# Kernel tuning notes

Measured on AMD Instinct MI355X. Metric: run time of the kernel, lower is better.

## Reference

```python
import jax, jax.numpy as jnp
import numpy as np
from jax import lax

B, N, C = 8, 4096, 384
HEADS = 6


def setup_inputs() -> dict:
    key = jax.random.key(0)
    ks = jax.random.split(key, 10)
    d = C // HEADS
    return {
        "x": jax.random.normal(ks[0], (B, N, C), jnp.float32),
        "q_w": jax.random.normal(ks[1], (C, C), jnp.float32) * 0.02,
        "q_b": jnp.zeros((C,), jnp.float32),
        "kv_w": jax.random.normal(ks[2], (2 * C, C), jnp.float32) * 0.02,
        "kv_b": jnp.zeros((2 * C,), jnp.float32),
        "fc_w": jax.random.normal(ks[3], (9, 3 * HEADS, 1, 1), jnp.float32) * 0.33,
        "fc_b": jnp.zeros((9,), jnp.float32),
        "dep_w": jax.random.normal(ks[4], (C, 9, 3, 3), jnp.float32) * 0.15,
        "dep_b": jnp.zeros((C,), jnp.float32),
        "ln_g": jnp.ones((C,), jnp.float32),
        "ln_b": jnp.zeros((C,), jnp.float32),
        "proj_w": jax.random.normal(ks[5], (C, C), jnp.float32) * 0.02,
        "proj_b": jnp.zeros((C,), jnp.float32),
        "H": 64,
        "W": 64,
    }


def reference(x, q_w, q_b, kv_w, kv_b, fc_w, fc_b, dep_w, dep_b, ln_g, ln_b, proj_w, proj_b, H, W):
    b, n, c = x.shape
    heads = fc_w.shape[1] // 3
    d = c // heads  # head dim == conv groups
    # QKV projections
    q = x @ q_w.T + q_b                                    # [B,N,C]
    kv = x @ kv_w.T + kv_b                                 # [B,N,2C]
    kv_ = kv.reshape(b, n, 2 * heads, d).transpose(0, 2, 1, 3)  # [B,2h,N,d]
    qh = q.reshape(b, n, heads, d).transpose(0, 2, 1, 3)        # [B,h,N,d]
    qkv = jnp.concatenate([qh, kv_], axis=1)               # [B,3h,N,d]
    # faithful torch reshape (row-major reinterpret), then permute
    f_all = qkv.reshape(b, n, 3 * heads, d).transpose(0, 2, 1, 3)  # [B,3h,N,d]
    # 1x1 conv over channel dim (fc): [B,9,N,d]
    f_conv = jnp.einsum('oi,bind->bond', fc_w[:, :, 0, 0], f_all) + fc_b[None, :, None, None]
    # [B,9,N,d] -> [B,d,9,N] -> [B,9*d,H,W] (d-major channel order, matches torch)
    f_conv = f_conv.transpose(0, 3, 1, 2).reshape(b, 9 * d, H, W)
    # grouped depthwise-style conv: in=9*d, out=C, groups=d
    out = lax.conv_general_dilated(
        f_conv, dep_w, window_strides=(1, 1), padding=[(1, 1), (1, 1)],
        dimension_numbers=('NCHW', 'OIHW', 'NCHW'), feature_group_count=d)
    out = out + dep_b[None, :, None, None]                 # [B,C,H,W]
    out = out.transpose(0, 2, 3, 1).reshape(b, n, c)       # [B,N,C]
    # LayerNorm over C
    mu = jnp.mean(out, axis=-1, keepdims=True)
    var = jnp.mean((out - mu) ** 2, axis=-1, keepdims=True)
    out = (out - mu) * lax.rsqrt(var + 1e-5) * ln_g + ln_b
    # exact GELU (torch nn.GELU default)
    out = jax.nn.gelu(out, approximate=False)
    return out @ proj_w.T + proj_b
```

## Files before the change

### kernel.cpp

```cpp
#include <hip/hip_runtime.h>
#include <hip/hip_bf16.h>

typedef __hip_bfloat16 bf16;
typedef __attribute__((ext_vector_type(8))) short bfx8;
typedef __attribute__((ext_vector_type(4))) short bfx4;
typedef __attribute__((ext_vector_type(4))) float fx4;
typedef __attribute__((ext_vector_type(4))) int ix4;
typedef __attribute__((ext_vector_type(2))) int ix2;

#define KD 384
#define CH 384

__device__ __forceinline__ float bf2f(bf16 v) { return __bfloat162float(v); }
__device__ __forceinline__ bf16 f2bf(float v) { return __float2bfloat16(v); }
__device__ __forceinline__ int pk2(float x, float y) {
    return (int)(((unsigned)__bfloat16_as_ushort(__float2bfloat16(y)) << 16) |
                 (unsigned)__bfloat16_as_ushort(__float2bfloat16(x)));
}
__device__ __forceinline__ float lo16(int u) { return __uint_as_float((unsigned)u << 16); }
__device__ __forceinline__ float hi16(int u) { return __uint_as_float((unsigned)u & 0xffff0000u); }

typedef const __attribute__((address_space(1))) void gvoid;
typedef __attribute__((address_space(3))) void lvoid;
__device__ __forceinline__ void gload16(const void* g, void* l) {
    __builtin_amdgcn_global_load_lds((gvoid*)g, (lvoid*)l, 16, 0, 0);
}

__global__ __launch_bounds__(256) void cast_kernel(
    const float* __restrict__ x, const float* __restrict__ qw,
    const float* __restrict__ kvw, const float* __restrict__ pw,
    bf16* __restrict__ dst)
{
    const int i = blockIdx.x * 256 + threadIdx.x;
    const float* s; int off;
    if (i < 3145728)      { s = x;   off = i; }
    else if (i < 3182592) { s = qw;  off = i - 3145728; }
    else if (i < 3256320) { s = kvw; off = i - 3182592; }
    else                  { s = pw;  off = i - 3256320; }
    const fx4 v = *(const fx4*)(s + (size_t)off * 4);
    const ix2 p = (ix2){pk2(v[0], v[1]), pk2(v[2], v[3])};
    *(ix2*)(void*)(dst + (size_t)i * 4) = p;
}

template <int MODE>
__global__ __launch_bounds__(256) void gemm_tile(
    const bf16* __restrict__ A, const bf16* __restrict__ B0,
    const bf16* __restrict__ B1, const float* __restrict__ bias0,
    const float* __restrict__ bias1, void* __restrict__ outv)
{
    constexpr int NT = (MODE == 0) ? 9 : 3;
    const int tid  = threadIdx.x;
    const int wave = tid >> 6, lane = tid & 63;

    const int f = blockIdx.x;
    const int xcd = f & 7, idx = f >> 3;
    const int mi = idx / NT, nt = idx - mi * NT;
    const int m0 = (xcd + (mi << 3)) * 128;
    const int n0 = nt * 128;

    const bf16* Bsrc;
    const float* bsrc;
    int boff;
    if constexpr (MODE == 0) {
        if (n0 >= CH) { Bsrc = B1 + (size_t)(n0 - CH) * KD; bsrc = bias1; boff = n0 - CH; }
        else          { Bsrc = B0 + (size_t)n0 * KD;        bsrc = bias0; boff = n0; }
    } else {
        Bsrc = B0 + (size_t)n0 * KD; bsrc = bias0; boff = n0;
    }

    const int wm = (wave & 1) * 64, wn = (wave >> 1) * 64;
    const int r16 = lane & 15, quad = lane >> 4;
    const int sr = lane >> 2, sseg = lane & 3;

    constexpr int SMEM = (MODE == 0) ? 17408 : 16384;
    __shared__ __align__(16) char smem[SMEM];
    bf16* As = (bf16*)smem;
    bf16* Bs = (bf16*)(smem + 8192);

    fx4 acc[4][4];
#pragma unroll
    for (int i = 0; i < 4; ++i)
#pragma unroll
        for (int j = 0; j < 4; ++j) acc[i][j] = (fx4){0.f, 0.f, 0.f, 0.f};

    for (int kt = 0; kt < KD; kt += 32) {
        __syncthreads();
#pragma unroll
        for (int ii = 0; ii < 2; ++ii) {
            const int c = ii * 4 + wave;
            const int r = c * 16 + sr;
            gload16(A + (size_t)(m0 + r) * KD + kt + sseg * 8, (char*)As + c * 1024);
            gload16(Bsrc + (size_t)r * KD + kt + sseg * 8, (char*)Bs + c * 1024);
        }
        __syncthreads();

        bfx8 af[4], bfr[4];
#pragma unroll
        for (int t = 0; t < 4; ++t) {
            af[t]  = *(const bfx8*)(const void*)(As + (wm + t * 16 + r16) * 32 + quad * 8);
            bfr[t] = *(const bfx8*)(const void*)(Bs + (wn + t * 16 + r16) * 32 + quad * 8);
        }
#pragma unroll
        for (int i = 0; i < 4; ++i)
#pragma unroll
            for (int j = 0; j < 4; ++j)
                acc[i][j] = __builtin_amdgcn_mfma_f32_16x16x32_bf16(
                    af[i], bfr[j], acc[i][j], 0, 0, 0);
    }

    if constexpr (MODE == 0) {
        bf16* tr = (bf16*)smem;
        const int bb = m0 >> 12, mbase = m0 & 4095;
#pragma unroll
        for (int half = 0; half < 2; ++half) {
            __syncthreads();
            if ((wave >> 1) == half) {
#pragma unroll
                for (int j = 0; j < 4; ++j) {
                    const int ocl = j * 16 + r16;
                    const float bv = bsrc[boff + wn + j * 16 + r16];
#pragma unroll
                    for (int i = 0; i < 4; ++i) {
                        const int m_loc = wm + i * 16 + quad * 4;
                        const ix2 pr = (ix2){
                            pk2(acc[i][j][0] + bv, acc[i][j][1] + bv),
                            pk2(acc[i][j][2] + bv, acc[i][j][3] + bv)};
                        *(ix2*)(void*)(tr + ocl * 136 + m_loc) = pr;
                    }
                }
            }
            __syncthreads();
            bf16* outp = (bf16*)outv;
            for (int u = tid; u < 1024; u += 256) {
                const int ocl = u >> 4, seg = u & 15;
                const int oc = n0 + half * 64 + ocl;
                const int g = oc >> 6, dd = oc & 63;
                const ix4 val = *(const ix4*)(const void*)(tr + ocl * 136 + seg * 8);
                const size_t dst = (((size_t)(bb * 64 + dd)) * 18 + g) * 4096 + mbase + seg * 8;
                *(ix4*)(void*)(outp + dst) = val;
            }
        }
    } else {
#pragma unroll
        for (int j = 0; j < 4; ++j) {
            const int oc = n0 + wn + j * 16 + r16;
            const float bv = bsrc[boff + wn + j * 16 + r16];
#pragma unroll
            for (int i = 0; i < 4; ++i) {
#pragma unroll
                for (int v = 0; v < 4; ++v) {
                    const int r = m0 + wm + i * 16 + quad * 4 + v;
                    ((float*)outv)[(size_t)r * CH + oc] = acc[i][j][v] + bv;
                }
            }
        }
    }
}

__global__ __launch_bounds__(256) void fcconv_kernel(
    const bf16* __restrict__ qkv2, const float* __restrict__ fc_w,
    const float* __restrict__ fc_b, const float* __restrict__ dep_w,
    const float* __restrict__ dep_b, bf16* __restrict__ cvo)
{
    const int tid = threadIdx.x;
    const int q = blockIdx.x, dd = blockIdx.y, b = blockIdx.z;
    const int h0 = q * 16;

    __shared__ bf16 img[9 * 18 * 68];

    const bf16* qb = qkv2 + ((size_t)(b * 64 + dd)) * 73728;

    for (int p = tid; p < 18 * 66; p += 256) {
        const int r = p / 66, cc = p - r * 66;
        const int h = h0 - 1 + r, wg = cc - 1;
        float s[9];
        if (h >= 0 && h < 64 && wg >= 0 && wg < 64) {
            const int n = h * 64 + wg;
            const int* tp = (const int*)(const void*)(qb + (size_t)n * 18);
            float xv[18];
#pragma unroll
            for (int k = 0; k < 9; ++k) {
                const int u = tp[k];
                xv[2 * k]     = lo16(u);
                xv[2 * k + 1] = hi16(u);
            }
#pragma unroll
            for (int o = 0; o < 9; ++o) {
                float t = fc_b[o];
#pragma unroll
                for (int i = 0; i < 18; ++i) t += fc_w[o * 18 + i] * xv[i];
                s[o] = t;
            }
        } else {
#pragma unroll
            for (int o = 0; o < 9; ++o) s[o] = 0.f;
        }
#pragma unroll
        for (int o = 0; o < 9; ++o) img[(o * 18 + r) * 68 + cc] = f2bf(s[o]);
    }
    __syncthreads();

    const int r_out = tid >> 4;
    const int w0 = (tid & 15) * 4;

    float acc[6][4];
#pragma unroll
    for (int oc = 0; oc < 6; ++oc) {
        const float bv = dep_b[dd * 6 + oc];
#pragma unroll
        for (int k = 0; k < 4; ++k) acc[oc][k] = bv;
    }

    const float* wbase = dep_w + (size_t)dd * 486;
    for (int j = 0; j < 9; ++j) {
        float wj[6][9];
#pragma unroll
        for (int oc = 0; oc < 6; ++oc)
#pragma unroll
            for (int t = 0; t < 9; ++t) wj[oc][t] = wbase[oc * 81 + j * 9 + t];
#pragma unroll
        for (int dy = 0; dy < 3; ++dy) {
            const bf16* rp = img + (j * 18 + r_out + dy) * 68 + w0;
            const ix2 d01 = *(const ix2*)(const void*)rp;
            const int d2 = *(const int*)(const void*)(rp + 4);
            const float x0 = lo16(d01[0]), x1 = hi16(d01[0]);
            const float x2 = lo16(d01[1]), x3 = hi16(d01[1]);
            const float x4 = lo16(d2),     x5 = hi16(d2);
#pragma unroll
            for (int oc = 0; oc < 6; ++oc) {
                const float k0 = wj[oc][dy * 3], k1 = wj[oc][dy * 3 + 1], k2 = wj[oc][dy * 3 + 2];
                acc[oc][0] += k0 * x0 + k1 * x1 + k2 * x2;
                acc[oc][1] += k0 * x1 + k1 * x2 + k2 * x3;
                acc[oc][2] += k0 * x2 + k1 * x3 + k2 * x4;
                acc[oc][3] += k0 * x3 + k1 * x4 + k2 * x5;
            }
        }
    }

#pragma unroll
    for (int oc = 0; oc < 6; ++oc) {
        const size_t base =
            ((size_t)(b * 384 + dd * 6 + oc)) * 4096 + (h0 + r_out) * 64 + w0;
        const ix2 pr = (ix2){pk2(acc[oc][0], acc[oc][1]), pk2(acc[oc][2], acc[oc][3])};
        *(ix2*)(void*)(cvo + base) = pr;
    }
}

__global__ __launch_bounds__(256) void ln_gelu_kernel(
    const bf16* __restrict__ cvo, const float* __restrict__ ln_g,
    const float* __restrict__ ln_b, bf16* __restrict__ gel)
{
    const int tid = threadIdx.x;
    const int n0 = blockIdx.x * 32;
    const int b  = blockIdx.y;

    __shared__ float tile[384 * 33];
    __shared__ float ps[32 * 9], pq[32 * 9];
    __shared__ float mu_s[32], inv_s[32];

    const bf16* src = cvo + (size_t)b * 384 * 4096;
    for (int v = tid; v < 384 * 8; v += 256) {
        const int oc = v >> 3, j = v & 7;
        const ix2 d = *(const ix2*)(const void*)(src + (size_t)oc * 4096 + n0 + j * 4);
        float* tp = tile + oc * 33 + j * 4;
        tp[0] = lo16(d[0]); tp[1] = hi16(d[0]);
        tp[2] = lo16(d[1]); tp[3] = hi16(d[1]);
    }
    __syncthreads();

    {
        const int nl = tid & 31, sl = tid >> 5;
        float s = 0.f, q = 0.f;
        for (int oc = sl * 48; oc < sl * 48 + 48; ++oc) {
            const float xv = tile[oc * 33 + nl];
            s += xv; q += xv * xv;
        }
        ps[nl * 9 + sl] = s; pq[nl * 9 + sl] = q;
    }
    __syncthreads();
    if (tid < 32) {
        float s = 0.f, q = 0.f;
        for (int k = 0; k < 8; ++k) { s += ps[tid * 9 + k]; q += pq[tid * 9 + k]; }
        const float mu = s * (1.f / 384.f);
        const float var = q * (1.f / 384.f) - mu * mu;
        mu_s[tid] = mu; inv_s[tid] = rsqrtf(var + 1e-5f);
    }
    __syncthreads();

    for (int v = tid; v < 192 * 32; v += 256) {
        const int oc2 = v % 192, nl = v / 192;
        const int oc = oc2 * 2;
        const float mu = mu_s[nl], inv = inv_s[nl];
        const float x0 = tile[oc * 33 + nl];
        const float x1 = tile[(oc + 1) * 33 + nl];
        const float y0 = (x0 - mu) * inv * ln_g[oc] + ln_b[oc];
        const float y1 = (x1 - mu) * inv * ln_g[oc + 1] + ln_b[oc + 1];
        const float g0 = 0.5f * y0 * (1.f + erff(y0 * 0.70710678118f));
        const float g1 = 0.5f * y1 * (1.f + erff(y1 * 0.70710678118f));
        *(int*)(void*)(gel + ((size_t)b * 4096 + n0 + nl) * 384 + oc) = pk2(g0, g1);
    }
}

extern "C" void kernel_launch(void* const* d_in, const int* in_sizes, int n_in,
                              void* d_out, int out_size, void* d_ws, size_t ws_size,
                              hipStream_t stream)
{
    const float* x      = (const float*)d_in[0];
    const float* q_w    = (const float*)d_in[1];
    const float* q_b    = (const float*)d_in[2];
    const float* kv_w   = (const float*)d_in[3];
    const float* kv_b   = (const float*)d_in[4];
    const float* fc_w   = (const float*)d_in[5];
    const float* fc_b   = (const float*)d_in[6];
    const float* dep_w  = (const float*)d_in[7];
    const float* dep_b  = (const float*)d_in[8];
    const float* ln_g   = (const float*)d_in[9];
    const float* ln_b   = (const float*)d_in[10];
    const float* proj_w = (const float*)d_in[11];
    const float* proj_b = (const float*)d_in[12];

    char* ws = (char*)d_ws;
    bf16*  castspan = (bf16*)ws;
    bf16*  xb     = castspan;
    bf16*  qwb    = castspan + 12582912;
    bf16*  kvwb   = castspan + 12730368;
    bf16*  projwb = castspan + 13025280;
    bf16*  qkv2   = (bf16*)(ws + 26345472);
    bf16*  cvo    = (bf16*)(ws + 101842944);
    bf16*  gel    = (bf16*)(ws + 127008768);

    cast_kernel<<<dim3(12864), 256, 0, stream>>>(x, q_w, kv_w, proj_w, castspan);
    gemm_tile<0><<<dim3(2304), 256, 0, stream>>>(xb, qwb, kvwb, q_b, kv_b, qkv2);
    fcconv_kernel<<<dim3(4, 64, 8), 256, 0, stream>>>(qkv2, fc_w, fc_b, dep_w,
                                                      dep_b, cvo);
    ln_gelu_kernel<<<dim3(128, 8), 256, 0, stream>>>(cvo, ln_g, ln_b, gel);
    gemm_tile<1><<<dim3(768), 256, 0, stream>>>(gel, projwb, nullptr, proj_b,
                                                nullptr, d_out);
}
```

Before: 270.6 us.

## Compute grouped 3x3 conv with MFMA bf16 instead of scalar FMAs

Replaces the per-thread scalar FMA loop of the grouped 3x3 conv with an MFMA 16x16x32 bf16 formulation. The 6 output channels are padded to 16 rows of the A fragment, and the 27 (j,dy) taps are padded to 32 along K, with one MFMA per dx. The B fragment is gathered from the LDS image with scalar 16-bit loads. This targets the conv's ALU cost, but most of the matrix unit work is padding, the weights are rounded to bf16, and the gathered LDS reads with strided stores may limit any gain.

Result: faster. 262.1 us (-3.1%).

```diff
diff --git a/kernel.cpp b/kernel.cpp
--- a/kernel.cpp
+++ b/kernel.cpp
@@ -200,49 +200,65 @@
     }
     __syncthreads();
 
-    const int r_out = tid >> 4;
-    const int w0 = (tid & 15) * 4;
-
-    float acc[6][4];
-#pragma unroll
-    for (int oc = 0; oc < 6; ++oc) {
-        const float bv = dep_b[dd * 6 + oc];
-#pragma unroll
-        for (int k = 0; k < 4; ++k) acc[oc][k] = bv;
-    }
-
-    const float* wbase = dep_w + (size_t)dd * 486;
-    for (int j = 0; j < 9; ++j) {
-        float wj[6][9];
-#pragma unroll
-        for (int oc = 0; oc < 6; ++oc)
-#pragma unroll
-            for (int t = 0; t < 9; ++t) wj[oc][t] = wbase[oc * 81 + j * 9 + t];
-#pragma unroll
-        for (int dy = 0; dy < 3; ++dy) {
-            const bf16* rp = img + (j * 18 + r_out + dy) * 68 + w0;
-            const ix2 d01 = *(const ix2*)(const void*)rp;
-            const int d2 = *(const int*)(const void*)(rp + 4);
-            const float x0 = lo16(d01[0]), x1 = hi16(d01[0]);
-            const float x2 = lo16(d01[1]), x3 = hi16(d01[1]);
-            const float x4 = lo16(d2),     x5 = hi16(d2);
-#pragma unroll
-            for (int oc = 0; oc < 6; ++oc) {
-                const float k0 = wj[oc][dy * 3], k1 = wj[oc][dy * 3 + 1], k2 = wj[oc][dy * 3 + 2];
-                acc[oc][0] += k0 * x0 + k1 * x1 + k2 * x2;
-                acc[oc][1] += k0 * x1 + k1 * x2 + k2 * x3;
-                acc[oc][2] += k0 * x2 + k1 * x3 + k2 * x4;
-                acc[oc][3] += k0 * x3 + k1 * x4 + k2 * x5;
-            }
-        }
-    }
-
-#pragma unroll
-    for (int oc = 0; oc < 6; ++oc) {
-        const size_t base =
-            ((size_t)(b * 384 + dd * 6 + oc)) * 4096 + (h0 + r_out) * 64 + w0;
-        const ix2 pr = (ix2){pk2(acc[oc][0], acc[oc][1]), pk2(acc[oc][2], acc[oc][3])};
-        *(ix2*)(void*)(cvo + base) = pr;
+    const int wave = tid >> 6, lane = tid & 63;
+    const int col = lane & 15, quad = lane >> 4;
+
+    bfx8 af3[3];
+    int joff[8];
+    {
+        const float* wsrc = dep_w + (size_t)dd * 486 + (size_t)col * 81;
+#pragma unroll
+        for (int dx = 0; dx < 3; ++dx) {
+            short tmp[8];
+#pragma unroll
+            for (int e = 0; e < 8; ++e) {
+                const int k = quad * 8 + e;
+                const int j = k / 3, dy = k - j * 3;
+                float v = 0.f;
+                if (col < 6 && k < 27) v = wsrc[j * 9 + dy * 3 + dx];
+                tmp[e] = (short)__bfloat16_as_ushort(f2bf(v));
+                if (dx == 0) joff[e] = (k < 27) ? (j * 1224 + dy * 68) : 0;
+            }
+            af3[dx] = (bfx8){tmp[0], tmp[1], tmp[2], tmp[3],
+                             tmp[4], tmp[5], tmp[6], tmp[7]};
+        }
+    }
+    float fb[4];
+#pragma unroll
+    for (int i = 0; i < 4; ++i) {
+        const int oc = quad * 4 + i;
+        fb[i] = (oc < 6) ? dep_b[dd * 6 + oc] : 0.f;
+    }
+
+    const unsigned short* img_s = (const unsigned short*)(const void*)img;
+    bf16* outb = cvo + ((size_t)(b * 384 + dd * 6)) * 4096;
+
+    for (int t = wave; t < 64; t += 4) {
+        const int rr = t >> 2, wg2 = t & 3;
+        const int w = wg2 * 16 + col;
+        const int base = rr * 68 + w;
+        int ve[8];
+#pragma unroll
+        for (int e = 0; e < 8; ++e) ve[e] = base + joff[e];
+
+        fx4 acc = (fx4){0.f, 0.f, 0.f, 0.f};
+#pragma unroll
+        for (int dx = 0; dx < 3; ++dx) {
+            short tmp[8];
+#pragma unroll
+            for (int e = 0; e < 8; ++e) tmp[e] = (short)img_s[ve[e] + dx];
+            const bfx8 bfrag = (bfx8){tmp[0], tmp[1], tmp[2], tmp[3],
+                                      tmp[4], tmp[5], tmp[6], tmp[7]};
+            acc = __builtin_amdgcn_mfma_f32_16x16x32_bf16(af3[dx], bfrag, acc,
+                                                          0, 0, 0);
+        }
+
+        const int n = (h0 + rr) * 64 + w;
+#pragma unroll
+        for (int i = 0; i < 4; ++i) {
+            const int oc = quad * 4 + i;
+            if (oc < 6) outb[(size_t)oc * 4096 + n] = f2bf(acc[i] + fb[i]);
+        }
     }
 }
 
```
